# Performance work log

Measured on AMD Instinct MI355X. Metric: run time of the kernel, lower is better.

Reference implementation:

```python
import jax, jax.numpy as jnp
import numpy as np

B, S, E, A = 4, 2048, 1024, 1024


def setup_inputs() -> dict:
    key = jax.random.key(0)
    k0, k1, k2, k3 = jax.random.split(key, 4)
    scale = 1.0 / np.sqrt(E)
    return {
        "embeds": jax.random.normal(k0, (B, S, E), dtype=jnp.float32),
        "Wq": jax.random.normal(k1, (E, A), dtype=jnp.float32) * scale,
        "Wk": jax.random.normal(k2, (E, A), dtype=jnp.float32) * scale,
        "Wv": jax.random.normal(k3, (E, A), dtype=jnp.float32) * scale,
    }


def reference(embeds, Wq, Wk, Wv):
    # projections: [B, S, A]
    q = jnp.einsum("bse,ea->bsa", embeds, Wq)
    k = jnp.einsum("bse,ea->bsa", embeds, Wk)
    v = jnp.einsum("bse,ea->bsa", embeds, Wv)
    attn_dim = k.shape[-1]
    # scores: [B, S, S], scaled by sqrt(attention_dim)
    scores = jnp.einsum("bqa,bka->bqk", q, k) / jnp.sqrt(
        jnp.asarray(attn_dim, dtype=q.dtype)
    )
    seq = scores.shape[-1]
    causal = jnp.tril(jnp.ones((seq, seq), dtype=bool))  # [S, S]
    scores = jnp.where(causal[None, :, :], scores, -jnp.inf)
    probs = jax.nn.softmax(scores, axis=-1)
    return jnp.einsum("bqk,bka->bqa", probs, v)
```

## Files before the change

### kernel.cpp

```cpp
#include <hip/hip_runtime.h>
#include <hip/hip_bf16.h>

#define DI __device__ __forceinline__

typedef __attribute__((ext_vector_type(8))) __bf16 bf16x8;
typedef __attribute__((ext_vector_type(4))) float f32x4;
typedef __attribute__((ext_vector_type(8))) short short8;
typedef __attribute__((ext_vector_type(4))) short short4v;
typedef unsigned short u16;

static constexpr int BB = 4, SS = 2048, EE = 1024, AA = 1024;

DI float bf2f(u16 u) { unsigned v = ((unsigned)u) << 16; float f; __builtin_memcpy(&f, &v, 4); return f; }
DI u16 f2bf(float f) { __hip_bfloat16 h = __float2bfloat16(f); u16 u; __builtin_memcpy(&u, &h, 2); return u; }

DI void gload16(const void* g, void* l) {
  __builtin_amdgcn_global_load_lds((const __attribute__((address_space(1))) void*)g,
                                   (__attribute__((address_space(3))) void*)l, 16, 0, 0);
}

DI int xcd_swz(int lin, int nwg) {
  int cpx = nwg >> 3;
  return (lin & 7) * cpx + (lin >> 3);
}

DI bf16x8 read_frag(const char* lds, int R, int c) {
  return *(const bf16x8*)(lds + R * 128 + ((c ^ (R & 7)) << 4));
}

__global__ __launch_bounds__(512, 2) void k_proj4(const u16* __restrict__ Xb, const u16* __restrict__ Wt,
                                                  u16* __restrict__ Qb, u16* __restrict__ Vt) {
  __shared__ __align__(16) char smem[131072];
  const int tid = threadIdx.x, lane = tid & 63, wid = tid >> 6;
  const int wr = wid >> 2, wc = wid & 3;
  const int lane15 = lane & 15, lhi = lane >> 4;
  const int lin = blockIdx.x;
  const int jj = lin >> 3;
  const int mt = (lin & 7) * 4 + (jj & 3);
  const int nt = jj >> 2;
  const u16* Ap = Xb + (size_t)mt * 256 * EE;
  const u16* Bp = Wt + (size_t)nt * 256 * EE;

  auto stageA = [&](int t, char* buf) {
#pragma unroll
    for (int i = 0; i < 4; ++i) {
      int blk = i * 8 + wid;
      int r = blk * 8 + (lane >> 3);
      int c = (lane & 7) ^ (r & 7);
      gload16((const char*)(Ap + (size_t)t * 64 + (size_t)r * EE) + c * 16, buf + blk * 1024);
    }
  };
  auto stageB = [&](int t, char* buf) {
#pragma unroll
    for (int i = 0; i < 4; ++i) {
      int blk = i * 8 + wid;
      int r = blk * 8 + (lane >> 3);
      int c = (lane & 7) ^ (r & 7);
      gload16((const char*)(Bp + (size_t)t * 64 + (size_t)r * EE) + c * 16, buf + 32768 + blk * 1024);
    }
  };

  f32x4 acc[8][4];
#pragma unroll
  for (int i = 0; i < 8; ++i)
#pragma unroll
    for (int j = 0; j < 4; ++j) acc[i][j] = (f32x4)0.f;

  stageA(0, smem); stageB(0, smem);
  asm volatile("s_waitcnt vmcnt(0)" ::: "memory");
  __builtin_amdgcn_s_barrier();

#pragma unroll 1
  for (int t = 0; t < 16; ++t) {
    const char* As = smem + (t & 1) * 65536;
    const char* Bs = As + 32768;
    char* nxt = smem + ((t & 1) ^ 1) * 65536;
    const bool st = (t + 1 < 16);
    bf16x8 bfr[4][2];

#pragma unroll
    for (int q = 0; q < 4; ++q) {
      if (q == 0) {
#pragma unroll
        for (int ni = 0; ni < 4; ++ni)
#pragma unroll
          for (int ks = 0; ks < 2; ++ks)
            bfr[ni][ks] = read_frag(Bs, wc * 64 + ni * 16 + lane15, ks * 4 + lhi);
      }
      bf16x8 af[2][2];
#pragma unroll
      for (int m2 = 0; m2 < 2; ++m2)
#pragma unroll
        for (int ks = 0; ks < 2; ++ks)
          af[m2][ks] = read_frag(As, wr * 128 + (q * 2 + m2) * 16 + lane15, ks * 4 + lhi);
      if (q == 0 && st) stageA(t + 1, nxt);
      if (q == 1 && st) stageB(t + 1, nxt);
      __builtin_amdgcn_s_barrier();
      asm volatile("s_waitcnt lgkmcnt(0)" ::: "memory");
      __builtin_amdgcn_sched_barrier(0);
      __builtin_amdgcn_s_setprio(1);
#pragma unroll
      for (int m2 = 0; m2 < 2; ++m2)
#pragma unroll
        for (int ni = 0; ni < 4; ++ni)
#pragma unroll
          for (int ks = 0; ks < 2; ++ks)
            acc[q * 2 + m2][ni] =
                __builtin_amdgcn_mfma_f32_16x16x32_bf16(af[m2][ks], bfr[ni][ks], acc[q * 2 + m2][ni], 0, 0, 0);
      __builtin_amdgcn_s_setprio(0);
      __builtin_amdgcn_sched_barrier(0);
      if (q == 3) asm volatile("s_waitcnt vmcnt(0)" ::: "memory");
      __builtin_amdgcn_s_barrier();
    }
  }

  if (nt < 8) {
    const int w = nt >> 2;
    u16* Op = Qb + (size_t)w * ((size_t)BB * SS * AA);
    const int r0 = mt * 256 + wr * 128;
    const int c0 = (nt & 3) * 256 + wc * 64;
#pragma unroll
    for (int mi = 0; mi < 8; ++mi)
#pragma unroll
      for (int ni = 0; ni < 4; ++ni)
#pragma unroll
        for (int r = 0; r < 4; ++r) {
          int row = r0 + mi * 16 + lhi * 4 + r;
          int col = c0 + ni * 16 + lane15;
          Op[(size_t)row * AA + col] = f2bf(acc[mi][ni][r]);
        }
  } else {
    const int r0 = mt * 256 + wr * 128;
    const int c0 = (nt - 8) * 256 + wc * 64;
#pragma unroll
    for (int mi = 0; mi < 8; ++mi) {
      const int grow = r0 + mi * 16 + lhi * 4;
      const int b = grow >> 11, s = grow & 2047;
#pragma unroll
      for (int ni = 0; ni < 4; ++ni) {
        const int col = c0 + ni * 16 + lane15;
        short4v o;
#pragma unroll
        for (int r = 0; r < 4; ++r) o[r] = (short)f2bf(acc[mi][ni][r]);
        *(short4v*)(Vt + (size_t)b * AA * SS + (size_t)col * SS + s) = o;
      }
    }
  }
}

DI void stage_tile(const u16* g, int ld, char* lds, int wid, int lane) {
#pragma unroll
  for (int i = 0; i < 4; ++i) {
    int blk = i * 4 + wid;
    int r = blk * 8 + (lane >> 3);
    int c = (lane & 7) ^ (r & 7);
    gload16((const char*)(g + (size_t)r * ld) + c * 16, lds + blk * 1024);
  }
}

DI void gemm_tile(const u16* Ap, int lda, const u16* Bp, int ldb, int ksteps,
                  char* As, char* Bs, f32x4 acc[4][4]) {
  const int tid = threadIdx.x, lane = tid & 63, wid = tid >> 6;
  const int wr = wid >> 1, wc = wid & 1;
  for (int ks = 0; ks < ksteps; ++ks) {
    __syncthreads();
    stage_tile(Ap + (size_t)ks * 64, lda, As, wid, lane);
    stage_tile(Bp + (size_t)ks * 64, ldb, Bs, wid, lane);
    asm volatile("s_waitcnt vmcnt(0)" ::: "memory");
    __syncthreads();
#pragma unroll
    for (int ksub = 0; ksub < 2; ++ksub) {
      const int c = ksub * 4 + (lane >> 4);
      bf16x8 af[4], bfr[4];
#pragma unroll
      for (int mi = 0; mi < 4; ++mi) af[mi] = read_frag(As, wr * 64 + mi * 16 + (lane & 15), c);
#pragma unroll
      for (int ni = 0; ni < 4; ++ni) bfr[ni] = read_frag(Bs, wc * 64 + ni * 16 + (lane & 15), c);
#pragma unroll
      for (int mi = 0; mi < 4; ++mi)
#pragma unroll
        for (int ni = 0; ni < 4; ++ni)
          acc[mi][ni] = __builtin_amdgcn_mfma_f32_16x16x32_bf16(af[mi], bfr[ni], acc[mi][ni], 0, 0, 0);
    }
  }
}

__global__ __launch_bounds__(256) void k_prep(const float* __restrict__ X, const float* __restrict__ Wq,
                                              const float* __restrict__ Wk, const float* __restrict__ Wv,
                                              u16* __restrict__ Xb, u16* __restrict__ Wt,
                                              float* __restrict__ rowsum) {
  __shared__ float t[64][65];
  const int bid = blockIdx.x;
  if (bid < 8192) {
    if (bid < 32) rowsum[bid * 256 + threadIdx.x] = 0.f;
    size_t i = ((size_t)bid * 256 + threadIdx.x) * 4;
    f32x4 f = *(const f32x4*)(X + i);
    short4v o;
#pragma unroll
    for (int j = 0; j < 4; ++j) o[j] = (short)f2bf(f[j]);
    *(short4v*)(Xb + i) = o;
  } else {
    const int bx = bid - 8192;
    const int w = bx >> 8, rem = bx & 255;
    const int k0 = (rem & 15) * 64, n0 = (rem >> 4) * 64;
    const float* W = (w == 0) ? Wq : ((w == 1) ? Wk : Wv);
    u16* Wo = Wt + (size_t)w * EE * AA;
    const int tx = threadIdx.x & 63, ty = threadIdx.x >> 6;
#pragma unroll
    for (int r = 0; r < 16; ++r) {
      int k = r * 4 + ty;
      t[k][tx] = W[(size_t)(k0 + k) * AA + n0 + tx];
    }
    __syncthreads();
#pragma unroll
    for (int r = 0; r < 16; ++r) {
      int n = r * 4 + ty;
      Wo[(size_t)(n0 + n) * EE + k0 + tx] = f2bf(t[tx][n]);
    }
  }
}

__global__ __launch_bounds__(256) void k_scores(const u16* __restrict__ Q, const u16* __restrict__ K,
                                                u16* __restrict__ Sc, float* __restrict__ rowsum) {
  __shared__ __align__(16) char smem[32768];
  const int wg = xcd_swz(blockIdx.x, 544);
  const int b = wg / 136, t = wg % 136;
  int i = (int)((sqrtf(8.f * t + 1.f) - 1.f) * 0.5f);
  while ((i + 1) * (i + 2) / 2 <= t) ++i;
  while (i * (i + 1) / 2 > t) --i;
  const int j = t - i * (i + 1) / 2;
  const u16* Ap = Q + (size_t)b * SS * AA + (size_t)i * 128 * AA;
  const u16* Bp = K + (size_t)b * SS * AA + (size_t)j * 128 * AA;
  u16* Op = Sc + (size_t)b * SS * SS;
  float* rs = rowsum + (size_t)b * SS;
  f32x4 acc[4][4];
#pragma unroll
  for (int x = 0; x < 4; ++x)
#pragma unroll
    for (int y = 0; y < 4; ++y) acc[x][y] = (f32x4)0.f;
  gemm_tile(Ap, AA, Bp, AA, AA / 64, smem, smem + 16384, acc);
  const int lane = threadIdx.x & 63, wid = threadIdx.x >> 6;
  const int r0 = i * 128 + (wid >> 1) * 64, c0 = j * 128 + (wid & 1) * 64;
#pragma unroll
  for (int mi = 0; mi < 4; ++mi)
#pragma unroll
    for (int r = 0; r < 4; ++r) {
      const int row = r0 + mi * 16 + ((lane >> 4) << 2) + r;
      float psum = 0.f;
#pragma unroll
      for (int ni = 0; ni < 4; ++ni) {
        const int col = c0 + ni * 16 + (lane & 15);
        float e = (col <= row) ? __expf(acc[mi][ni][r] * 0.03125f) : 0.f;
        psum += e;
        Op[(size_t)row * SS + col] = f2bf(e);
      }
      psum += __shfl_xor(psum, 1, 16);
      psum += __shfl_xor(psum, 2, 16);
      psum += __shfl_xor(psum, 4, 16);
      psum += __shfl_xor(psum, 8, 16);
      if ((lane & 15) == 0) atomicAdd(&rs[row], psum);
    }
}

__global__ __launch_bounds__(256) void k_pv(const u16* __restrict__ Sc, const u16* __restrict__ Vt,
                                            const float* __restrict__ rowsum, float* __restrict__ Out) {
  __shared__ __align__(16) char smem[32768];
  const int lin = blockIdx.x;
  const int x = lin & 7;
  const int j = lin >> 3;
  const int b = j >> 4, half = (j >> 3) & 1, nt = j & 7;
  const int i = half ? (15 - x) : x;
  const u16* Ap = Sc + (size_t)b * SS * SS + (size_t)i * 128 * SS;
  const u16* Bp = Vt + (size_t)b * AA * SS + (size_t)nt * 128 * SS;
  const float* rs = rowsum + (size_t)b * SS;
  float* Op = Out + (size_t)b * SS * AA;
  f32x4 acc[4][4];
#pragma unroll
  for (int p = 0; p < 4; ++p)
#pragma unroll
    for (int q = 0; q < 4; ++q) acc[p][q] = (f32x4)0.f;
  gemm_tile(Ap, SS, Bp, SS, 2 * (i + 1), smem, smem + 16384, acc);
  const int lane = threadIdx.x & 63, wid = threadIdx.x >> 6;
  const int r0 = i * 128 + (wid >> 1) * 64, c0 = nt * 128 + (wid & 1) * 64;
#pragma unroll
  for (int mi = 0; mi < 4; ++mi)
#pragma unroll
    for (int r = 0; r < 4; ++r) {
      const int row = r0 + mi * 16 + ((lane >> 4) << 2) + r;
      const float inv = 1.f / rs[row];
#pragma unroll
      for (int ni = 0; ni < 4; ++ni) {
        const int col = c0 + ni * 16 + (lane & 15);
        Op[(size_t)row * AA + col] = acc[mi][ni][r] * inv;
      }
    }
}

extern "C" void kernel_launch(void* const* d_in, const int* in_sizes, int n_in,
                              void* d_out, int out_size, void* d_ws, size_t ws_size,
                              hipStream_t stream) {
  const float* X  = (const float*)d_in[0];
  const float* Wq = (const float*)d_in[1];
  const float* Wk = (const float*)d_in[2];
  const float* Wv = (const float*)d_in[3];
  float* Out = (float*)d_out;
  char* ws = (char*)d_ws;
  u16* Xb = (u16*)ws;
  u16* Wt = (u16*)(ws + (16u << 20));
  u16* Qb = (u16*)(ws + (22u << 20));
  u16* Kb = (u16*)(ws + (38u << 20));
  u16* Vt = (u16*)(ws + (70u << 20));
  u16* Sc = (u16*)(ws + (86u << 20));
  float* rowsum = (float*)(ws + (118u << 20));
  (void)Kb;

  k_prep<<<dim3(8192 + 768), 256, 0, stream>>>(X, Wq, Wk, Wv, Xb, Wt, rowsum);
  k_proj4<<<dim3(384), 512, 0, stream>>>(Xb, Wt, Qb, Vt);
  k_scores<<<dim3(136 * BB), 256, 0, stream>>>(Qb, Kb, Sc, rowsum);
  k_pv<<<dim3(512), 256, 0, stream>>>(Sc, Vt, rowsum, Out);
}
```

Before: 167.4 us.

## Retile projection GEMM to 256x192 tiles and double-buffer shared gemm_tile

The fused QKV projection kernel now uses 256x192 output tiles, giving 512 workgroups instead of 384, with a unified epilogue that routes columns to Q/K or transposed V. The shared gemm_tile used by the scores and PV kernels becomes double-buffered, prefetching the next K-slice into a second LDS buffer while MFMAs run on the current one. This removes a barrier per step and overlaps global loads with compute. The cost is doubled LDS per workgroup in those kernels, 64KB instead of 32KB, which can lower occupancy.

After: 142.8 us. 14.7% less time.

```diff
diff --git a/kernel.cpp b/kernel.cpp
--- a/kernel.cpp
+++ b/kernel.cpp
@@ -28,9 +28,9 @@
   return *(const bf16x8*)(lds + R * 128 + ((c ^ (R & 7)) << 4));
 }
 
-__global__ __launch_bounds__(512, 2) void k_proj4(const u16* __restrict__ Xb, const u16* __restrict__ Wt,
+__global__ __launch_bounds__(512, 2) void k_proj5(const u16* __restrict__ Xb, const u16* __restrict__ Wt,
                                                   u16* __restrict__ Qb, u16* __restrict__ Vt) {
-  __shared__ __align__(16) char smem[131072];
+  __shared__ __align__(16) char smem[114688];
   const int tid = threadIdx.x, lane = tid & 63, wid = tid >> 6;
   const int wr = wid >> 2, wc = wid & 3;
   const int lane15 = lane & 15, lhi = lane >> 4;
@@ -39,7 +39,7 @@
   const int mt = (lin & 7) * 4 + (jj & 3);
   const int nt = jj >> 2;
   const u16* Ap = Xb + (size_t)mt * 256 * EE;
-  const u16* Bp = Wt + (size_t)nt * 256 * EE;
+  const u16* Bp = Wt + (size_t)nt * 192 * EE;
 
   auto stageA = [&](int t, char* buf) {
 #pragma unroll
@@ -52,7 +52,7 @@
   };
   auto stageB = [&](int t, char* buf) {
 #pragma unroll
-    for (int i = 0; i < 4; ++i) {
+    for (int i = 0; i < 3; ++i) {
       int blk = i * 8 + wid;
       int r = blk * 8 + (lane >> 3);
       int c = (lane & 7) ^ (r & 7);
@@ -60,11 +60,11 @@
     }
   };
 
-  f32x4 acc[8][4];
+  f32x4 acc[8][3];
 #pragma unroll
   for (int i = 0; i < 8; ++i)
 #pragma unroll
-    for (int j = 0; j < 4; ++j) acc[i][j] = (f32x4)0.f;
+    for (int j = 0; j < 3; ++j) acc[i][j] = (f32x4)0.f;
 
   stageA(0, smem); stageB(0, smem);
   asm volatile("s_waitcnt vmcnt(0)" ::: "memory");
@@ -72,20 +72,20 @@
 
 #pragma unroll 1
   for (int t = 0; t < 16; ++t) {
-    const char* As = smem + (t & 1) * 65536;
+    const char* As = smem + (t & 1) * 57344;
     const char* Bs = As + 32768;
-    char* nxt = smem + ((t & 1) ^ 1) * 65536;
+    char* nxt = smem + ((t & 1) ^ 1) * 57344;
     const bool st = (t + 1 < 16);
-    bf16x8 bfr[4][2];
+    bf16x8 bfr[3][2];
 
 #pragma unroll
     for (int q = 0; q < 4; ++q) {
       if (q == 0) {
 #pragma unroll
-        for (int ni = 0; ni < 4; ++ni)
+        for (int ni = 0; ni < 3; ++ni)
 #pragma unroll
           for (int ks = 0; ks < 2; ++ks)
-            bfr[ni][ks] = read_frag(Bs, wc * 64 + ni * 16 + lane15, ks * 4 + lhi);
+            bfr[ni][ks] = read_frag(Bs, wc * 48 + ni * 16 + lane15, ks * 4 + lhi);
       }
       bf16x8 af[2][2];
 #pragma unroll
@@ -102,7 +102,7 @@
 #pragma unroll
       for (int m2 = 0; m2 < 2; ++m2)
 #pragma unroll
-        for (int ni = 0; ni < 4; ++ni)
+        for (int ni = 0; ni < 3; ++ni)
 #pragma unroll
           for (int ks = 0; ks < 2; ++ks)
             acc[q * 2 + m2][ni] =
@@ -114,35 +114,26 @@
     }
   }
 
-  if (nt < 8) {
-    const int w = nt >> 2;
-    u16* Op = Qb + (size_t)w * ((size_t)BB * SS * AA);
-    const int r0 = mt * 256 + wr * 128;
-    const int c0 = (nt & 3) * 256 + wc * 64;
-#pragma unroll
-    for (int mi = 0; mi < 8; ++mi)
-#pragma unroll
-      for (int ni = 0; ni < 4; ++ni)
-#pragma unroll
-        for (int r = 0; r < 4; ++r) {
-          int row = r0 + mi * 16 + lhi * 4 + r;
-          int col = c0 + ni * 16 + lane15;
-          Op[(size_t)row * AA + col] = f2bf(acc[mi][ni][r]);
-        }
-  } else {
-    const int r0 = mt * 256 + wr * 128;
-    const int c0 = (nt - 8) * 256 + wc * 64;
-#pragma unroll
-    for (int mi = 0; mi < 8; ++mi) {
-      const int grow = r0 + mi * 16 + lhi * 4;
-      const int b = grow >> 11, s = grow & 2047;
-#pragma unroll
-      for (int ni = 0; ni < 4; ++ni) {
-        const int col = c0 + ni * 16 + lane15;
+  const int r0 = mt * 256 + wr * 128;
+  const int c0 = nt * 192 + wc * 48;
+#pragma unroll
+  for (int mi = 0; mi < 8; ++mi) {
+    const int grow = r0 + mi * 16 + lhi * 4;
+    const int b = grow >> 11, s = grow & 2047;
+#pragma unroll
+    for (int ni = 0; ni < 3; ++ni) {
+      const int col = c0 + ni * 16 + lane15;
+      if (col < 2048) {
+        u16* base = Qb + (size_t)(col >> 10) * ((size_t)BB * SS * AA);
+#pragma unroll
+        for (int r = 0; r < 4; ++r)
+          base[(size_t)(grow + r) * AA + (col & 1023)] = f2bf(acc[mi][ni][r]);
+      } else {
+        const int a = col - 2048;
         short4v o;
 #pragma unroll
         for (int r = 0; r < 4; ++r) o[r] = (short)f2bf(acc[mi][ni][r]);
-        *(short4v*)(Vt + (size_t)b * AA * SS + (size_t)col * SS + s) = o;
+        *(short4v*)(Vt + (size_t)b * AA * SS + (size_t)a * SS + s) = o;
       }
     }
   }
@@ -159,15 +150,22 @@
 }
 
 DI void gemm_tile(const u16* Ap, int lda, const u16* Bp, int ldb, int ksteps,
-                  char* As, char* Bs, f32x4 acc[4][4]) {
+                  char* smem, f32x4 acc[4][4]) {
   const int tid = threadIdx.x, lane = tid & 63, wid = tid >> 6;
   const int wr = wid >> 1, wc = wid & 1;
+  stage_tile(Ap, lda, smem, wid, lane);
+  stage_tile(Bp, ldb, smem + 16384, wid, lane);
+  asm volatile("s_waitcnt vmcnt(0)" ::: "memory");
+  __syncthreads();
+#pragma unroll 1
   for (int ks = 0; ks < ksteps; ++ks) {
-    __syncthreads();
-    stage_tile(Ap + (size_t)ks * 64, lda, As, wid, lane);
-    stage_tile(Bp + (size_t)ks * 64, ldb, Bs, wid, lane);
-    asm volatile("s_waitcnt vmcnt(0)" ::: "memory");
-    __syncthreads();
+    const char* As = smem + (ks & 1) * 32768;
+    const char* Bs = As + 16384;
+    char* nxt = smem + ((ks & 1) ^ 1) * 32768;
+    if (ks + 1 < ksteps) {
+      stage_tile(Ap + (size_t)(ks + 1) * 64, lda, nxt, wid, lane);
+      stage_tile(Bp + (size_t)(ks + 1) * 64, ldb, nxt + 16384, wid, lane);
+    }
 #pragma unroll
     for (int ksub = 0; ksub < 2; ++ksub) {
       const int c = ksub * 4 + (lane >> 4);
@@ -182,6 +180,8 @@
         for (int ni = 0; ni < 4; ++ni)
           acc[mi][ni] = __builtin_amdgcn_mfma_f32_16x16x32_bf16(af[mi], bfr[ni], acc[mi][ni], 0, 0, 0);
     }
+    if (ks + 1 < ksteps) asm volatile("s_waitcnt vmcnt(0)" ::: "memory");
+    __syncthreads();
   }
 }
 
@@ -222,7 +222,7 @@
 
 __global__ __launch_bounds__(256) void k_scores(const u16* __restrict__ Q, const u16* __restrict__ K,
                                                 u16* __restrict__ Sc, float* __restrict__ rowsum) {
-  __shared__ __align__(16) char smem[32768];
+  __shared__ __align__(16) char smem[65536];
   const int wg = xcd_swz(blockIdx.x, 544);
   const int b = wg / 136, t = wg % 136;
   int i = (int)((sqrtf(8.f * t + 1.f) - 1.f) * 0.5f);
@@ -238,7 +238,7 @@
   for (int x = 0; x < 4; ++x)
 #pragma unroll
     for (int y = 0; y < 4; ++y) acc[x][y] = (f32x4)0.f;
-  gemm_tile(Ap, AA, Bp, AA, AA / 64, smem, smem + 16384, acc);
+  gemm_tile(Ap, AA, Bp, AA, AA / 64, smem, acc);
   const int lane = threadIdx.x & 63, wid = threadIdx.x >> 6;
   const int r0 = i * 128 + (wid >> 1) * 64, c0 = j * 128 + (wid & 1) * 64;
 #pragma unroll
@@ -264,7 +264,7 @@
 
 __global__ __launch_bounds__(256) void k_pv(const u16* __restrict__ Sc, const u16* __restrict__ Vt,
                                             const float* __restrict__ rowsum, float* __restrict__ Out) {
-  __shared__ __align__(16) char smem[32768];
+  __shared__ __align__(16) char smem[65536];
   const int lin = blockIdx.x;
   const int x = lin & 7;
   const int j = lin >> 3;
@@ -279,7 +279,7 @@
   for (int p = 0; p < 4; ++p)
 #pragma unroll
     for (int q = 0; q < 4; ++q) acc[p][q] = (f32x4)0.f;
-  gemm_tile(Ap, SS, Bp, SS, 2 * (i + 1), smem, smem + 16384, acc);
+  gemm_tile(Ap, SS, Bp, SS, 2 * (i + 1), smem, acc);
   const int lane = threadIdx.x & 63, wid = threadIdx.x >> 6;
   const int r0 = i * 128 + (wid >> 1) * 64, c0 = nt * 128 + (wid & 1) * 64;
 #pragma unroll
@@ -312,10 +312,9 @@
   u16* Vt = (u16*)(ws + (70u << 20));
   u16* Sc = (u16*)(ws + (86u << 20));
   float* rowsum = (float*)(ws + (118u << 20));
-  (void)Kb;
 
   k_prep<<<dim3(8192 + 768), 256, 0, stream>>>(X, Wq, Wk, Wv, Xb, Wt, rowsum);
-  k_proj4<<<dim3(384), 512, 0, stream>>>(Xb, Wt, Qb, Vt);
+  k_proj5<<<dim3(512), 512, 0, stream>>>(Xb, Wt, Qb, Vt);
   k_scores<<<dim3(136 * BB), 256, 0, stream>>>(Qb, Kb, Sc, rowsum);
   k_pv<<<dim3(512), 256, 0, stream>>>(Sc, Vt, rowsum, Out);
 }
```
